# Optimization experiments

Measured on AMD Instinct MI355X. Metric: run time of the kernel, lower is better.

Reference implementation:

```python
import jax, jax.numpy as jnp
import numpy as np
from jax import lax

KH, KW = 4, 10  # kernel_size default in Deconw


def setup_inputs() -> dict:
    key = jax.random.key(0)
    k1, k2 = jax.random.split(key)
    B, H, Wd, C = 16, 128, 512, 64
    x = jax.random.normal(k1, (B, H, Wd, C), dtype=jnp.float32)
    # stacked per-channel Conv2DTranspose kernels (filters=1 each) and biases
    W = jax.random.normal(k2, (KH, KW, C), dtype=jnp.float32) * 0.05
    b = jnp.zeros((C,), dtype=jnp.float32)
    return {"x": x, "W": W, "b": b}


def reference(x, W, b):
    # Depthwise transposed conv, stride 1, 'valid' padding.
    # Conv2DTranspose with stride 1 == full correlation with spatially-flipped
    # kernel, i.e. pad input by (kh-1, kw-1) on each side then plain conv.
    B, H, Wd, C = x.shape
    kh, kw, _ = W.shape
    xp = jnp.pad(x, ((0, 0), (kh - 1, kh - 1), (kw - 1, kw - 1), (0, 0)))
    # HWIO kernel, one input channel per group, C groups -> fused depthwise op
    kern = jnp.flip(W, axis=(0, 1)).reshape(kh, kw, 1, C)
    y = lax.conv_general_dilated(
        xp, kern,
        window_strides=(1, 1), padding="VALID",
        dimension_numbers=("NHWC", "HWIO", "NHWC"),
        feature_group_count=C,
    )  # [B, H+kh-1, W+kw-1, C]
    y = y + b  # per-channel bias
    # original: stack over channels then transpose (1,0,2,3,4) -> [B, C, Ho, Wo, 1]
    return jnp.transpose(y, (0, 3, 1, 2))[..., None]
```

## Files before the change

### kernel.cpp

```cpp
#include <hip/hip_runtime.h>


#define H_IN 128
#define W_IN 512
#define C_CH 64
#define KH 4
#define KW 10
#define OHT 131
#define OWT 521
#define OW_TILE 64
#define OH_TILE 16
#define LSTRIDE 81
#define NW_STRIPS 9
#define NH_STRIPS 9

#define STAGE(IH)                                                          \
  {                                                                        \
    const int rowb = ((bN * H_IN + (IH)) * W_IN);                          \
    _Pragma("unroll")                                                      \
    for (int k = 0; k < 5; ++k) {                                          \
      const int f   = tid + 256 * k;                                       \
      const int iwl = f >> 4;                                              \
      const int c4  = f & 15;                                              \
      const int iw  = w0 - (KW - 1) + iwl;                                 \
      if (iw >= 0 && iw < W_IN)                                            \
        stg[k] = xf4[(rowb + iw) * (C_CH / 4) + c4];                       \
      else                                                                 \
        stg[k] = make_float4(0.f, 0.f, 0.f, 0.f);                          \
    }                                                                      \
  }

#define LDSWRITE(IH)                                                       \
  {                                                                        \
    float* Lb = lbuf[(IH) & 1];                                            \
    _Pragma("unroll")                                                      \
    for (int k = 0; k < 5; ++k) {                                          \
      const int f   = tid + 256 * k;                                       \
      const int iwl = f >> 4;                                              \
      const int c4  = (f & 15) * 4;                                        \
      Lb[(c4 + 0) * LSTRIDE + iwl] = stg[k].x;                             \
      Lb[(c4 + 1) * LSTRIDE + iwl] = stg[k].y;                             \
      Lb[(c4 + 2) * LSTRIDE + iwl] = stg[k].z;                             \
      Lb[(c4 + 3) * LSTRIDE + iwl] = stg[k].w;                             \
    }                                                                      \
  }

#define COMPUTE(IH, A0_, A1_, A2_, A3_)                                    \
  {                                                                        \
    const float* Lb = lbuf[(IH) & 1];                                      \
    float xv[25];                                                          \
    _Pragma("unroll")                                                      \
    for (int t = 0; t < 25; ++t) xv[t] = Lb[c * LSTRIDE + ws * 16 + t];    \
    _Pragma("unroll")                                                      \
    for (int q = 0; q < KW; ++q) {                                         \
      const float w0_ = wk[q];                                             \
      const float w1_ = wk[KW + q];                                        \
      const float w2_ = wk[2 * KW + q];                                    \
      const float w3_ = wk[3 * KW + q];                                    \
      _Pragma("unroll")                                                    \
      for (int s = 0; s < 16; ++s) {                                       \
        const float xvv = xv[s + (KW - 1) - q];                            \
        A0_[s] = fmaf(xvv, w0_, A0_[s]);                                   \
        A1_[s] = fmaf(xvv, w1_, A1_[s]);                                   \
        A2_[s] = fmaf(xvv, w2_, A2_[s]);                                   \
        A3_[s] = fmaf(xvv, w3_, A3_[s]);                                   \
      }                                                                    \
    }                                                                      \
  }

#define EMIT(IH, A0_)                                                      \
  {                                                                        \
    const int oh = (IH);                                                   \
    if (oh >= oh0 && oh <= ohMax) {                                        \
      float* orow = outg + ((bN * C_CH + c) * OHT + oh) * OWT + owBase;    \
      if (owBase + 15 < OWT) {                                             \
        _Pragma("unroll")                                                  \
        for (int s = 0; s < 16; ++s) orow[s] = A0_[s];                     \
      } else {                                                             \
        _Pragma("unroll")                                                  \
        for (int s = 0; s < 16; ++s)                                       \
          if (owBase + s < OWT) orow[s] = A0_[s];                          \
      }                                                                    \
    }                                                                      \
    _Pragma("unroll")                                                      \
    for (int s = 0; s < 16; ++s) A0_[s] = biasv;                           \
  }

#define STEP(A0_, A1_, A2_, A3_, IH)                                       \
  if ((IH) <= stepEnd) {                                                   \
    if ((IH) <= ihEnd) LDSWRITE(IH);                                       \
    __syncthreads();                                                       \
    if ((IH) + 1 <= ihEnd) STAGE((IH) + 1);                                \
    if ((IH) <= ihEnd) COMPUTE(IH, A0_, A1_, A2_, A3_);                    \
    EMIT(IH, A0_);                                                         \
  }

__global__ __launch_bounds__(256, 2) void deconw_kernel(
    const float* __restrict__ xg, const float* __restrict__ wg,
    const float* __restrict__ bg, float* __restrict__ outg)
{
    __shared__ float lbuf[2][C_CH * LSTRIDE];

    const int tid  = threadIdx.x;
    const int bid  = blockIdx.x;
    const int wsid = bid % NW_STRIPS;
    const int hsid = (bid / NW_STRIPS) % NH_STRIPS;
    const int bN   = bid / (NW_STRIPS * NH_STRIPS);

    const int w0  = wsid * OW_TILE;
    const int oh0 = hsid * OH_TILE;

    const int c      = tid >> 2;
    const int ws     = tid & 3;
    const int owBase = w0 + ws * 16;

    float wk[KH * KW];
#pragma unroll
    for (int i = 0; i < KH * KW; ++i) wk[i] = wg[i * C_CH + c];
    const float biasv = bg[c];

    const int ihStart = (oh0 - (KH - 1)) > 0 ? (oh0 - (KH - 1)) : 0;
    const int ihEnd   = (oh0 + OH_TILE - 1) < (H_IN - 1) ? (oh0 + OH_TILE - 1) : (H_IN - 1);
    const int stepEnd = ihEnd + (KH - 1);
    const int ohMax   = (oh0 + OH_TILE - 1) < (OHT - 1) ? (oh0 + OH_TILE - 1) : (OHT - 1);

    const float4* xf4 = (const float4*)xg;
    float4 stg[5];

    float R0[16], R1[16], R2[16], R3[16];
#pragma unroll
    for (int s = 0; s < 16; ++s) { R0[s] = biasv; R1[s] = biasv; R2[s] = biasv; R3[s] = biasv; }

    STAGE(ihStart);

    for (int ihb = ihStart; ihb <= stepEnd; ihb += 4) {
        STEP(R0, R1, R2, R3, ihb + 0);
        STEP(R1, R2, R3, R0, ihb + 1);
        STEP(R2, R3, R0, R1, ihb + 2);
        STEP(R3, R0, R1, R2, ihb + 3);
    }
}

extern "C" void kernel_launch(void* const* d_in, const int* in_sizes, int n_in,
                              void* d_out, int out_size, void* d_ws, size_t ws_size,
                              hipStream_t stream)
{
    const float* x = (const float*)d_in[0];
    const float* W = (const float*)d_in[1];
    const float* b = (const float*)d_in[2];
    float* out     = (float*)d_out;

    const int B = 16;
    dim3 grid(NW_STRIPS * NH_STRIPS * B);
    dim3 block(256);
    deconw_kernel<<<grid, block, 0, stream>>>(x, W, b, out);
}
```

Measured before the change: 1.413 ms.

## Stage output rows through LDS for coalesced nontemporal stores, remap workgroups across XCDs

Each thread's 16 finished output values are written to the idle LDS buffer. The block then transposes them so that each wave stores 64 contiguous output-width elements per channel row with nontemporal stores, replacing scattered 16-element per-thread row writes. Block IDs are remapped so that consecutive tiles land on the same XCD, and the step loop now ends at the last valid output row instead of running extra redundant steps. The cost is two extra barriers per emitted row, and the LDS buffer now serves both roles.

After: 1.463 ms. +3.6%, slower.

```diff
diff --git a/kernel.cpp b/kernel.cpp
--- a/kernel.cpp
+++ b/kernel.cpp
@@ -11,8 +11,10 @@
 #define OW_TILE 64
 #define OH_TILE 16
 #define LSTRIDE 81
+#define OSTRIDE 68
 #define NW_STRIPS 9
 #define NH_STRIPS 9
+#define NB 16
 
 #define STAGE(IH)                                                          \
   {                                                                        \
@@ -68,19 +70,25 @@
     }                                                                      \
   }
 
-#define EMIT(IH, A0_)                                                      \
+#define EMITSTORE(IH, A0_)                                                 \
   {                                                                        \
-    const int oh = (IH);                                                   \
-    if (oh >= oh0 && oh <= ohMax) {                                        \
-      float* orow = outg + ((bN * C_CH + c) * OHT + oh) * OWT + owBase;    \
-      if (owBase + 15 < OWT) {                                             \
+    if ((IH) >= oh0) {                                                     \
+      float* Ob = lbuf[((IH) + 1) & 1];                                    \
+      float4* Op = (float4*)&Ob[c * OSTRIDE + ws * 16];                    \
+      Op[0] = make_float4(A0_[0], A0_[1], A0_[2], A0_[3]);                 \
+      Op[1] = make_float4(A0_[4], A0_[5], A0_[6], A0_[7]);                 \
+      Op[2] = make_float4(A0_[8], A0_[9], A0_[10], A0_[11]);               \
+      Op[3] = make_float4(A0_[12], A0_[13], A0_[14], A0_[15]);             \
+      __syncthreads();                                                     \
+      if (owok) {                                                          \
+        float* orow = outg + ((bN * C_CH + wv * 16) * OHT + (IH)) * OWT    \
+                      + w0 + ln;                                           \
         _Pragma("unroll")                                                  \
-        for (int s = 0; s < 16; ++s) orow[s] = A0_[s];                     \
-      } else {                                                             \
-        _Pragma("unroll")                                                  \
-        for (int s = 0; s < 16; ++s)                                       \
-          if (owBase + s < OWT) orow[s] = A0_[s];                          \
+        for (int j = 0; j < 16; ++j)                                       \
+          __builtin_nontemporal_store(Ob[(wv * 16 + j) * OSTRIDE + ln],    \
+                                      &orow[j * OHT * OWT]);               \
       }                                                                    \
+      __syncthreads();                                                     \
     }                                                                      \
     _Pragma("unroll")                                                      \
     for (int s = 0; s < 16; ++s) A0_[s] = biasv;                           \
@@ -92,7 +100,7 @@
     __syncthreads();                                                       \
     if ((IH) + 1 <= ihEnd) STAGE((IH) + 1);                                \
     if ((IH) <= ihEnd) COMPUTE(IH, A0_, A1_, A2_, A3_);                    \
-    EMIT(IH, A0_);                                                         \
+    EMITSTORE(IH, A0_);                                                    \
   }
 
 __global__ __launch_bounds__(256, 2) void deconw_kernel(
@@ -101,8 +109,12 @@
 {
     __shared__ float lbuf[2][C_CH * LSTRIDE];
 
-    const int tid  = threadIdx.x;
-    const int bid  = blockIdx.x;
+    const int tid = threadIdx.x;
+
+    const int nwg = NW_STRIPS * NH_STRIPS * NB;
+    const int cpx = nwg >> 3;
+    const int bid = ((int)blockIdx.x & 7) * cpx + ((int)blockIdx.x >> 3);
+
     const int wsid = bid % NW_STRIPS;
     const int hsid = (bid / NW_STRIPS) % NH_STRIPS;
     const int bN   = bid / (NW_STRIPS * NH_STRIPS);
@@ -112,7 +124,9 @@
 
     const int c      = tid >> 2;
     const int ws     = tid & 3;
-    const int owBase = w0 + ws * 16;
+    const int wv     = tid >> 6;
+    const int ln     = tid & 63;
+    const bool owok  = (w0 + ln) < OWT;
 
     float wk[KH * KW];
 #pragma unroll
@@ -121,8 +135,8 @@
 
     const int ihStart = (oh0 - (KH - 1)) > 0 ? (oh0 - (KH - 1)) : 0;
     const int ihEnd   = (oh0 + OH_TILE - 1) < (H_IN - 1) ? (oh0 + OH_TILE - 1) : (H_IN - 1);
-    const int stepEnd = ihEnd + (KH - 1);
     const int ohMax   = (oh0 + OH_TILE - 1) < (OHT - 1) ? (oh0 + OH_TILE - 1) : (OHT - 1);
+    const int stepEnd = ohMax;
 
     const float4* xf4 = (const float4*)xg;
     float4 stg[5];
@@ -150,8 +164,7 @@
     const float* b = (const float*)d_in[2];
     float* out     = (float*)d_out;
 
-    const int B = 16;
-    dim3 grid(NW_STRIPS * NH_STRIPS * B);
+    dim3 grid(NW_STRIPS * NH_STRIPS * NB);
     dim3 block(256);
     deconw_kernel<<<grid, block, 0, stream>>>(x, W, b, out);
 }
```
